# Performance work log

Hardware: AMD Instinct MI355X
Metric: run time of the kernel (lower is better)

The kernel has to match this reference:

```python
import jax, jax.numpy as jnp
import numpy as np

DIM = 1024
HIDDEN = 2560  # multiple_of*(int(2*4*DIM/3)//multiple_of)
N_EXPERTS = 4
TOP_K = 2


def setup_inputs() -> dict:
    key = jax.random.key(0)
    ks = jax.random.split(key, 5)
    scale_d = 1.0 / np.sqrt(DIM)
    scale_h = 1.0 / np.sqrt(HIDDEN)
    x = jax.random.normal(ks[0], (8, 1024, DIM), dtype=jnp.float32)
    gate_w = jax.random.normal(ks[1], (N_EXPERTS, DIM), dtype=jnp.float32) * scale_d
    # torch Linear weight layout [out, in]; stacked over experts
    w1 = jax.random.normal(ks[2], (N_EXPERTS, HIDDEN, DIM), dtype=jnp.float32) * scale_d
    w3 = jax.random.normal(ks[3], (N_EXPERTS, HIDDEN, DIM), dtype=jnp.float32) * scale_d
    w2 = jax.random.normal(ks[4], (N_EXPERTS, DIM, HIDDEN), dtype=jnp.float32) * scale_h
    return {"x": x, "gate_w": gate_w, "w1": w1, "w2": w2, "w3": w3}


def reference(x, gate_w, w1, w2, w3):
    orig_shape = x.shape
    xf = x.reshape(-1, orig_shape[-1])  # [N, D]

    # gating: softmax -> top-k -> renormalize
    logits = jnp.einsum('nd,ed->ne', xf, gate_w)
    probs = jax.nn.softmax(logits, axis=-1)
    topk_w, topk_idx = jax.lax.top_k(probs, TOP_K)          # [N, K]
    topk_w = topk_w / jnp.sum(topk_w, axis=-1, keepdims=True)

    # per-token per-expert combine weight (0 if expert not selected)
    one_hot = jax.nn.one_hot(topk_idx, N_EXPERTS, dtype=xf.dtype)  # [N, K, E]
    comb = jnp.einsum('nk,nke->ne', topk_w, one_hot)               # [N, E]

    # dense per-expert SwiGLU FFN (4 experts), then weighted combine
    h1 = jnp.einsum('nd,ehd->neh', xf, w1)   # [N, E, H]
    h3 = jnp.einsum('nd,ehd->neh', xf, w3)
    h = jax.nn.silu(h1) * h3
    y = jnp.einsum('neh,edh->ned', h, w2)    # [N, E, D]
    out = jnp.einsum('ned,ne->nd', y, comb)  # [N, D]

    aux_loss = jnp.asarray(0.0, dtype=x.dtype)  # eval mode
    return out.reshape(orig_shape), aux_loss
```

## Files before the change

### kernel.cpp

```cpp
#include <hip/hip_runtime.h>

typedef unsigned short u16;
typedef unsigned int   u32;

#define DIM  1024
#define HID  2560
#define NTOK 8192
#define NEXP 4

#define BM 128
#define BN 128
#define BK 64
#define BN2 256

#define ESEG 4352
#define NROWS (NEXP * ESEG)

typedef __attribute__((ext_vector_type(8))) short bf16x8;
typedef __attribute__((ext_vector_type(4))) float f32x4;

__device__ __forceinline__ void async16(const void* g, void* l) {
  __builtin_amdgcn_global_load_lds((const __attribute__((address_space(1))) u32*)g,
                                   (__attribute__((address_space(3))) u32*)l,
                                   16, 0, 0);
}
__device__ __forceinline__ u16 f2bf(float f) {
  union { float f; u32 u; } c; c.f = f;
  u32 u = c.u;
  return (u16)((u + 0x7fffu + ((u >> 16) & 1u)) >> 16);
}
__device__ __forceinline__ ushort4 cvt4(float4 v) {
  ushort4 o; o.x = f2bf(v.x); o.y = f2bf(v.y); o.z = f2bf(v.z); o.w = f2bf(v.w);
  return o;
}

__global__ void zrt_kernel(int* __restrict__ rt) {
  if (threadIdx.x < 8) rt[threadIdx.x] = 0;
}

__global__ void cvt13_kernel(const float* __restrict__ w1, const float* __restrict__ w3,
                             u16* __restrict__ w1b, u16* __restrict__ w3b, int n4each) {
  int i = blockIdx.x * blockDim.x + threadIdx.x;
  if (i < n4each)
    ((ushort4*)w1b)[i] = cvt4(((const float4*)w1)[i]);
  else if (i < 2 * n4each)
    ((ushort4*)w3b)[i - n4each] = cvt4(((const float4*)w3)[i - n4each]);
}

__global__ void cvt2_kernel(const float* __restrict__ w2, u16* __restrict__ w2b, int n4) {
  int i = blockIdx.x * blockDim.x + threadIdx.x;
  if (i < n4) ((ushort4*)w2b)[i] = cvt4(((const float4*)w2)[i]);
}

__global__ void gate_kernel(const float* __restrict__ X, const float* __restrict__ GW,
                            float* __restrict__ comb, int* __restrict__ rt,
                            u16* __restrict__ Xb, int* __restrict__ idxpool,
                            float* __restrict__ out, int out_n) {
  __shared__ int s_pick[8];

  int gtid = blockIdx.x * blockDim.x + threadIdx.x;

  {
    int n4 = out_n >> 2;
    int stride = gridDim.x * blockDim.x;
    float4 z = {0.f, 0.f, 0.f, 0.f};
    for (int j = gtid; j < n4; j += stride) ((float4*)out)[j] = z;
    if (gtid == 0)
      for (int j = n4 << 2; j < out_n; ++j) out[j] = 0.f;
  }

  int tok  = gtid >> 6;
  int lane = gtid & 63;
  int widx = threadIdx.x >> 6;

  const float4* xv = (const float4*)(X + (size_t)tok * DIM + lane * 16);
  float4 x0 = xv[0], x1 = xv[1], x2 = xv[2], x3 = xv[3];

  ushort4* xb = (ushort4*)(Xb + (size_t)tok * DIM + lane * 16);
  xb[0] = cvt4(x0); xb[1] = cvt4(x1); xb[2] = cvt4(x2); xb[3] = cvt4(x3);

  float acc[NEXP];
#pragma unroll
  for (int e = 0; e < NEXP; ++e) {
    const float4* gv = (const float4*)(GW + e * DIM + lane * 16);
    float4 g0 = gv[0], g1 = gv[1], g2 = gv[2], g3 = gv[3];
    float s;
    s  = x0.x * g0.x + x0.y * g0.y + x0.z * g0.z + x0.w * g0.w;
    s += x1.x * g1.x + x1.y * g1.y + x1.z * g1.z + x1.w * g1.w;
    s += x2.x * g2.x + x2.y * g2.y + x2.z * g2.z + x2.w * g2.w;
    s += x3.x * g3.x + x3.y * g3.y + x3.z * g3.z + x3.w * g3.w;
    acc[e] = s;
  }
#pragma unroll
  for (int off = 32; off > 0; off >>= 1) {
#pragma unroll
    for (int e = 0; e < NEXP; ++e) acc[e] += __shfl_xor(acc[e], off);
  }
  if (lane == 0) {
    int i1 = 0;
#pragma unroll
    for (int e = 1; e < NEXP; ++e) if (acc[e] > acc[i1]) i1 = e;
    int i2 = -1;
#pragma unroll
    for (int e = 0; e < NEXP; ++e) {
      if (e == i1) continue;
      if (i2 < 0 || acc[e] > acc[i2]) i2 = e;
    }
    float m  = acc[i1];
    float e1 = __expf(acc[i1] - m), e2 = __expf(acc[i2] - m);
    float inv = 1.f / (e1 + e2);
    float w[NEXP] = {0.f, 0.f, 0.f, 0.f};
    w[i1] = e1 * inv; w[i2] = e2 * inv;
#pragma unroll
    for (int e = 0; e < NEXP; ++e) comb[(size_t)tok * NEXP + e] = w[e];
    s_pick[2 * widx]     = i1;
    s_pick[2 * widx + 1] = i2;
  }
  __syncthreads();

  if (threadIdx.x < 64) {
    int tid0 = threadIdx.x;
    int p  = (tid0 < 8) ? s_pick[tid0] : -1;
    int tk = blockIdx.x * 4 + (tid0 >> 1);
#pragma unroll
    for (int e = 0; e < NEXP; ++e) {
      unsigned long long b = __ballot(p == e);
      int cw = __popcll(b);
      if (cw) {
        int src = __ffsll((unsigned long long)b) - 1;
        int bp = 0;
        if (tid0 == src) bp = atomicAdd(&rt[4 + e], cw);
        bp = __shfl(bp, src);
        if (p == e) {
          int off = __popcll(b & ((1ull << tid0) - 1ull));
          int slot = bp + off;
          if (slot < ESEG) idxpool[e * ESEG + slot] = tk;
        }
      }
    }
  }
}


__global__ __launch_bounds__(256, 2) void ffn13_kernel(
    const u16* __restrict__ Xb, const u16* __restrict__ W1,
    const u16* __restrict__ W3, const float* __restrict__ combp,
    const int* __restrict__ idxpool, const int* __restrict__ rt,
    u16* __restrict__ Hpool) {
  const int e   = blockIdx.y >> 6;
  const int mb  = blockIdx.y & 63;
  int cnt = rt[4 + e]; if (cnt > ESEG) cnt = ESEG;
  const int m0  = mb * BM;
  if (m0 >= cnt) return;
  const int rbase = e * ESEG;
  const int n0    = blockIdx.x * BN;

  __shared__ __align__(16) u16 As [BM * BK];
  __shared__ __align__(16) u16 B1s[BN * BK];
  __shared__ __align__(16) u16 B3s[BN * BK];
  __shared__ float s_comb[BM];
  __shared__ int   s_idx [BM];

  const int tid  = threadIdx.x;
  const int wave = tid >> 6;
  const int lane = tid & 63;

  if (tid < BM) {
    int m = m0 + tid;
    int t = (m < cnt) ? idxpool[rbase + m] : 0;
    s_idx[tid]  = t;
    s_comb[tid] = combp[(size_t)t * NEXP + e];
  }
  __syncthreads();

  const u16* W1e = W1 + (size_t)e * HID * DIM;
  const u16* W3e = W3 + (size_t)e * HID * DIM;

  const int scc = (((tid & 7) ^ ((tid >> 3) & 7)) << 3);
  const int r0  = tid >> 3;
  const u16 *pA[4], *pB1[4], *pB3[4];
  int dsto[4];
#pragma unroll
  for (int q = 0; q < 4; ++q) {
    int row = r0 + 32 * q;
    pA[q]   = Xb  + (size_t)s_idx[row] * DIM + scc;
    pB1[q]  = W1e + (size_t)(n0 + row) * DIM + scc;
    pB3[q]  = W3e + (size_t)(n0 + row) * DIM + scc;
    dsto[q] = (tid + 256 * q) * 8;
  }

  const int wm = (wave >> 1) * 64, wn = (wave & 1) * 64;
  const int quad = lane >> 4, r = lane & 15;

  f32x4 acc1[4][4], acc3[4][4];
#pragma unroll
  for (int i = 0; i < 4; ++i)
#pragma unroll
    for (int j = 0; j < 4; ++j) {
      acc1[i][j] = (f32x4){0.f, 0.f, 0.f, 0.f};
      acc3[i][j] = (f32x4){0.f, 0.f, 0.f, 0.f};
    }

  for (int k0 = 0; k0 < DIM; k0 += BK) {
    __syncthreads();
#pragma unroll
    for (int q = 0; q < 4; ++q) { async16(pA[q],  &As [dsto[q]]); pA[q]  += BK; }
#pragma unroll
    for (int q = 0; q < 4; ++q) { async16(pB1[q], &B1s[dsto[q]]); pB1[q] += BK; }
#pragma unroll
    for (int q = 0; q < 4; ++q) { async16(pB3[q], &B3s[dsto[q]]); pB3[q] += BK; }
    __syncthreads();

#pragma unroll
    for (int s = 0; s < 2; ++s) {
      bf16x8 af[4], b1f[4], b3f[4];
#pragma unroll
      for (int i = 0; i < 4; ++i) {
        int row = wm + i * 16 + r;
        af[i] = *(const bf16x8*)&As[row * BK + ((((s << 2) + quad) ^ (row & 7)) << 3)];
      }
#pragma unroll
      for (int j = 0; j < 4; ++j) {
        int row = wn + j * 16 + r;
        int cc  = (((s << 2) + quad) ^ (row & 7)) << 3;
        b1f[j] = *(const bf16x8*)&B1s[row * BK + cc];
        b3f[j] = *(const bf16x8*)&B3s[row * BK + cc];
      }
#pragma unroll
      for (int i = 0; i < 4; ++i)
#pragma unroll
        for (int j = 0; j < 4; ++j) {
          acc1[i][j] = __builtin_amdgcn_mfma_f32_16x16x32_bf16(af[i], b1f[j], acc1[i][j], 0, 0, 0);
          acc3[i][j] = __builtin_amdgcn_mfma_f32_16x16x32_bf16(af[i], b3f[j], acc3[i][j], 0, 0, 0);
        }
    }
  }

#pragma unroll
  for (int i = 0; i < 4; ++i) {
    const int rowb = wm + i * 16 + quad * 4;
#pragma unroll
    for (int rr = 0; rr < 4; ++rr) {
      const float cw = s_comb[rowb + rr];
      u16* orow = Hpool + (size_t)(rbase + m0 + rowb + rr) * HID + n0 + wn + r;
#pragma unroll
      for (int j = 0; j < 4; ++j) {
        float v1v = acc1[i][j][rr];
        float v3v = acc3[i][j][rr];
        float sig = 1.f / (1.f + __expf(-v1v));
        orow[j * 16] = f2bf(cw * (v1v * sig * v3v));
      }
    }
  }
}

__global__ __launch_bounds__(256, 2) void ffn2_kernel(
    const u16* __restrict__ Hpool, const u16* __restrict__ W2b,
    const int* __restrict__ idxpool, const int* __restrict__ rt,
    float* __restrict__ Out) {
  __shared__ __align__(16) u16 As[BM * BK];
  __shared__ __align__(16) u16 Bs[BN2 * BK];
  __shared__ int s_idx[BM];

  const int x   = blockIdx.x & 7;
  const int e   = x >> 1;
  const int nbh = (x & 1) << 1;
  int cnt = rt[4 + e]; if (cnt > ESEG) cnt = ESEG;
  if (cnt == 0) return;
  const int Mb     = (cnt + BM - 1) >> 7;
  const int rbase  = e * ESEG;
  const int nunits = Mb << 1;

  const int tid  = threadIdx.x;
  const int wave = tid >> 6;
  const int lane = tid & 63;
  const int scc  = (((tid & 7) ^ ((tid >> 3) & 7)) << 3);
  const int r0   = tid >> 3;
  const int wm = (wave >> 1) * 64, wn = (wave & 1) * 128;
  const int quad = lane >> 4, r = lane & 15;

  for (int u = blockIdx.x >> 3; u < nunits; u += (gridDim.x >> 3)) {
    const int mb = u >> 1;
    const int nb = nbh + (u & 1);
    const int m0 = mb * BM;
    const int n0 = nb * BN2;

    __syncthreads();
    if (tid < BM) {
      int m = m0 + tid;
      s_idx[tid] = (m < cnt) ? idxpool[rbase + m] : -1;
    }

    const u16 *pa[4], *pb[8];
    int dstoA[4], dstoB[8];
#pragma unroll
    for (int q = 0; q < 4; ++q) {
      int row = r0 + 32 * q;
      pa[q]    = Hpool + (size_t)(rbase + m0 + row) * HID + scc;
      dstoA[q] = (tid + 256 * q) * 8;
    }
#pragma unroll
    for (int q = 0; q < 8; ++q) {
      int row = r0 + 32 * q;
      pb[q]    = W2b + ((size_t)e * DIM + n0 + row) * HID + scc;
      dstoB[q] = (tid + 256 * q) * 8;
    }

    f32x4 acc[4][8];
#pragma unroll
    for (int i = 0; i < 4; ++i)
#pragma unroll
      for (int j = 0; j < 8; ++j) acc[i][j] = (f32x4){0.f, 0.f, 0.f, 0.f};

    for (int k0 = 0; k0 < HID; k0 += BK) {
      __syncthreads();
#pragma unroll
      for (int q = 0; q < 4; ++q) { async16(pa[q], &As[dstoA[q]]); pa[q] += BK; }
#pragma unroll
      for (int q = 0; q < 8; ++q) { async16(pb[q], &Bs[dstoB[q]]); pb[q] += BK; }
      __syncthreads();

#pragma unroll
      for (int s = 0; s < 2; ++s) {
        bf16x8 af[4], bf[8];
#pragma unroll
        for (int i = 0; i < 4; ++i) {
          int row = wm + i * 16 + r;
          af[i] = *(const bf16x8*)&As[row * BK + ((((s << 2) + quad) ^ (row & 7)) << 3)];
        }
#pragma unroll
        for (int j = 0; j < 8; ++j) {
          int row = wn + j * 16 + r;
          bf[j] = *(const bf16x8*)&Bs[row * BK + ((((s << 2) + quad) ^ (row & 7)) << 3)];
        }
#pragma unroll
        for (int i = 0; i < 4; ++i)
#pragma unroll
          for (int j = 0; j < 8; ++j)
            acc[i][j] = __builtin_amdgcn_mfma_f32_16x16x32_bf16(af[i], bf[j], acc[i][j], 0, 0, 0);
      }
    }

#pragma unroll
    for (int i = 0; i < 4; ++i) {
      const int rowb = wm + i * 16 + quad * 4;
#pragma unroll
      for (int rr = 0; rr < 4; ++rr) {
        int tk = s_idx[rowb + rr];
        if (tk >= 0) {
          float* orow = Out + (size_t)tk * DIM + n0 + wn + r;
#pragma unroll
          for (int j = 0; j < 8; ++j) unsafeAtomicAdd(&orow[j * 16], acc[i][j][rr]);
        }
      }
    }
  }
}

__global__ void ws_marker_kernel(float* __restrict__ Out, float v) {
  if (threadIdx.x == 0 && blockIdx.x == 0) Out[0] = v;
}

extern "C" void kernel_launch(void* const* d_in, const int* in_sizes, int n_in,
                              void* d_out, int out_size, void* d_ws, size_t ws_size,
                              hipStream_t stream) {
  const float* x  = (const float*)d_in[0];
  const float* gw = (const float*)d_in[1];
  const float* w1 = (const float*)d_in[2];
  const float* w2 = (const float*)d_in[3];
  const float* w3 = (const float*)d_in[4];
  float* out = (float*)d_out;

  const size_t WELEMS = (size_t)NEXP * HID * DIM;
  const size_t WBYTES = WELEMS * sizeof(u16);
  char* ws = (char*)d_ws;
  float* comb    = (float*)ws;
  int*   rt      = (int*)(ws + 131072);
  int*   idxpool = (int*)(ws + 131072 + 128);
  u16*   w1b     = (u16*)(ws + 131072 + 128 + (size_t)NROWS * 4);
  u16*   w2b     = w1b;
  u16*   w3b     = w1b + WELEMS;
  u16*   Xb      = w3b + WELEMS;
  u16*   Hpool   = Xb + (size_t)NTOK * DIM;

  const size_t need = 131072 + 128 + (size_t)NROWS * 4 + 2 * WBYTES +
                      (size_t)NTOK * DIM * sizeof(u16) +
                      (size_t)NROWS * HID * sizeof(u16);
  if (ws_size < need) {
    float v = 5000.0f + (float)((ws_size >> 20) > 999 ? 999 : (ws_size >> 20));
    ws_marker_kernel<<<dim3(1), dim3(64), 0, stream>>>(out, v);
    return;
  }

  zrt_kernel<<<dim3(1), dim3(64), 0, stream>>>(rt);

  gate_kernel<<<dim3(NTOK / 4), dim3(256), 0, stream>>>(x, gw, comb, rt, Xb,
                                                        idxpool, out, out_size / 4);

  {
    int n4each = (int)(WELEMS / 4);
    cvt13_kernel<<<dim3((2 * n4each + 255) / 256), dim3(256), 0, stream>>>(
        w1, w3, w1b, w3b, n4each);
  }

  ffn13_kernel<<<dim3(HID / BN, 64 * NEXP), dim3(256), 0, stream>>>(
      Xb, w1b, w3b, comb, idxpool, rt, Hpool);

  {
    int n4 = (int)(WELEMS / 4);
    cvt2_kernel<<<dim3((n4 + 255) / 256), dim3(256), 0, stream>>>(w2, w2b, n4);
  }

  ffn2_kernel<<<dim3(512), dim3(256), 0, stream>>>(Hpool, w2b, idxpool, rt, out);
}
```

Before: 598.4 us.

## Double-buffer LDS tiles in ffn2 and shrink N tile to 128

```diff
diff --git a/kernel.cpp b/kernel.cpp
--- a/kernel.cpp
+++ b/kernel.cpp
@@ -11,7 +11,6 @@
 #define BM 128
 #define BN 128
 #define BK 64
-#define BN2 256
 
 #define ESEG 4352
 #define NROWS (NEXP * ESEG)
@@ -258,32 +257,32 @@
     const u16* __restrict__ Hpool, const u16* __restrict__ W2b,
     const int* __restrict__ idxpool, const int* __restrict__ rt,
     float* __restrict__ Out) {
-  __shared__ __align__(16) u16 As[BM * BK];
-  __shared__ __align__(16) u16 Bs[BN2 * BK];
+  __shared__ __align__(16) u16 As[2][BM * BK];
+  __shared__ __align__(16) u16 Bs[2][BN * BK];
   __shared__ int s_idx[BM];
 
   const int x   = blockIdx.x & 7;
   const int e   = x >> 1;
-  const int nbh = (x & 1) << 1;
+  const int nbh = (x & 1) << 2;
   int cnt = rt[4 + e]; if (cnt > ESEG) cnt = ESEG;
   if (cnt == 0) return;
   const int Mb     = (cnt + BM - 1) >> 7;
   const int rbase  = e * ESEG;
-  const int nunits = Mb << 1;
+  const int ntiles = Mb << 2;
 
   const int tid  = threadIdx.x;
   const int wave = tid >> 6;
   const int lane = tid & 63;
   const int scc  = (((tid & 7) ^ ((tid >> 3) & 7)) << 3);
   const int r0   = tid >> 3;
-  const int wm = (wave >> 1) * 64, wn = (wave & 1) * 128;
+  const int wm = (wave >> 1) * 64, wn = (wave & 1) * 64;
   const int quad = lane >> 4, r = lane & 15;
 
-  for (int u = blockIdx.x >> 3; u < nunits; u += (gridDim.x >> 3)) {
-    const int mb = u >> 1;
-    const int nb = nbh + (u & 1);
+  for (int t = blockIdx.x >> 3; t < ntiles; t += (gridDim.x >> 3)) {
+    const int mb = t >> 2;
+    const int nb = nbh + (t & 3);
     const int m0 = mb * BM;
-    const int n0 = nb * BN2;
+    const int n0 = nb * BN;
 
     __syncthreads();
     if (tid < BM) {
@@ -291,54 +290,59 @@
       s_idx[tid] = (m < cnt) ? idxpool[rbase + m] : -1;
     }
 
-    const u16 *pa[4], *pb[8];
-    int dstoA[4], dstoB[8];
+    const u16 *pa[4], *pb[4];
+    int dsto[4];
 #pragma unroll
     for (int q = 0; q < 4; ++q) {
       int row = r0 + 32 * q;
-      pa[q]    = Hpool + (size_t)(rbase + m0 + row) * HID + scc;
-      dstoA[q] = (tid + 256 * q) * 8;
-    }
-#pragma unroll
-    for (int q = 0; q < 8; ++q) {
-      int row = r0 + 32 * q;
-      pb[q]    = W2b + ((size_t)e * DIM + n0 + row) * HID + scc;
-      dstoB[q] = (tid + 256 * q) * 8;
-    }
-
-    f32x4 acc[4][8];
+      pa[q]   = Hpool + (size_t)(rbase + m0 + row) * HID + scc;
+      pb[q]   = W2b + ((size_t)e * DIM + n0 + row) * HID + scc;
+      dsto[q] = (tid + 256 * q) * 8;
+    }
+
+    f32x4 acc[4][4];
 #pragma unroll
     for (int i = 0; i < 4; ++i)
 #pragma unroll
-      for (int j = 0; j < 8; ++j) acc[i][j] = (f32x4){0.f, 0.f, 0.f, 0.f};
-
-    for (int k0 = 0; k0 < HID; k0 += BK) {
+      for (int j = 0; j < 4; ++j) acc[i][j] = (f32x4){0.f, 0.f, 0.f, 0.f};
+
+#pragma unroll
+    for (int q = 0; q < 4; ++q) { async16(pa[q], &As[0][dsto[q]]); pa[q] += BK; }
+#pragma unroll
+    for (int q = 0; q < 4; ++q) { async16(pb[q], &Bs[0][dsto[q]]); pb[q] += BK; }
+
+    int cur = 0;
+    const int NK = HID / BK;
+    for (int k = 0; k < NK; ++k) {
       __syncthreads();
-#pragma unroll
-      for (int q = 0; q < 4; ++q) { async16(pa[q], &As[dstoA[q]]); pa[q] += BK; }
-#pragma unroll
-      for (int q = 0; q < 8; ++q) { async16(pb[q], &Bs[dstoB[q]]); pb[q] += BK; }
-      __syncthreads();
+
+      if (k + 1 < NK) {
+#pragma unroll
+        for (int q = 0; q < 4; ++q) { async16(pa[q], &As[cur ^ 1][dsto[q]]); pa[q] += BK; }
+#pragma unroll
+        for (int q = 0; q < 4; ++q) { async16(pb[q], &Bs[cur ^ 1][dsto[q]]); pb[q] += BK; }
+      }
 
 #pragma unroll
       for (int s = 0; s < 2; ++s) {
-        bf16x8 af[4], bf[8];
+        bf16x8 af[4], bf[4];
 #pragma unroll
         for (int i = 0; i < 4; ++i) {
           int row = wm + i * 16 + r;
-          af[i] = *(const bf16x8*)&As[row * BK + ((((s << 2) + quad) ^ (row & 7)) << 3)];
+          af[i] = *(const bf16x8*)&As[cur][row * BK + ((((s << 2) + quad) ^ (row & 7)) << 3)];
         }
 #pragma unroll
-        for (int j = 0; j < 8; ++j) {
+        for (int j = 0; j < 4; ++j) {
           int row = wn + j * 16 + r;
-          bf[j] = *(const bf16x8*)&Bs[row * BK + ((((s << 2) + quad) ^ (row & 7)) << 3)];
+          bf[j] = *(const bf16x8*)&Bs[cur][row * BK + ((((s << 2) + quad) ^ (row & 7)) << 3)];
         }
 #pragma unroll
         for (int i = 0; i < 4; ++i)
 #pragma unroll
-          for (int j = 0; j < 8; ++j)
+          for (int j = 0; j < 4; ++j)
             acc[i][j] = __builtin_amdgcn_mfma_f32_16x16x32_bf16(af[i], bf[j], acc[i][j], 0, 0, 0);
       }
+      cur ^= 1;
     }
 
 #pragma unroll
@@ -350,7 +354,7 @@
         if (tk >= 0) {
           float* orow = Out + (size_t)tk * DIM + n0 + wn + r;
 #pragma unroll
-          for (int j = 0; j < 8; ++j) unsafeAtomicAdd(&orow[j * 16], acc[i][j][rr]);
+          for (int j = 0; j < 4; ++j) unsafeAtomicAdd(&orow[j * 16], acc[i][j][rr]);
         }
       }
     }
@@ -411,5 +415,5 @@
     cvt2_kernel<<<dim3((n4 + 255) / 256), dim3(256), 0, stream>>>(w2, w2b, n4);
   }
 
-  ffn2_kernel<<<dim3(512), dim3(256), 0, stream>>>(Hpool, w2b, idxpool, rt, out);
-}
+  ffn2_kernel<<<dim3(2048), dim3(256), 0, stream>>>(Hpool, w2b, idxpool, rt, out);
+}
```

After: 619.8 us. 3.6% more time.
